# Performance work log

Hardware: AMD Instinct MI355X
Metric: run time of the kernel (lower is better)

## Reference

```python
import jax, jax.numpy as jnp
import numpy as np

DIM = 1024
D_STATE = 16
D_CONV = 4
EXPAND = 2
D_INNER = DIM * EXPAND
DT_RANK = 64  # ceil(1024/16)
N_EXP = 8
TOP_K = 2
HID = DIM * 2
B, T = 2, 2048
EPS = 1e-5


def setup_inputs() -> dict:
    key = jax.random.key(0)
    ks = jax.random.split(key, 16)
    s = 0.02
    # dt bias init (softplus-inverse of dt in [1e-3, 1e-1]) as in the torch code
    dt_init = jnp.exp(jax.random.uniform(ks[0], (D_INNER,)) * (np.log(0.1) - np.log(0.001)) + np.log(0.001))
    dt_proj_b = dt_init + jnp.log(-jnp.expm1(-dt_init))
    A_log = jnp.broadcast_to(jnp.log(jnp.arange(1, D_STATE + 1, dtype=jnp.float32))[None, :], (D_INNER, D_STATE))
    return {
        "x": jax.random.normal(ks[1], (B, T, DIM), jnp.float32),
        "ssm_state": jnp.zeros((B, D_INNER, D_STATE), jnp.float32),
        "conv_state": jnp.zeros((B, D_INNER, D_CONV - 1), jnp.float32),
        "ln1_s": jnp.ones((DIM,), jnp.float32), "ln1_b": jnp.zeros((DIM,), jnp.float32),
        "ln2_s": jnp.ones((DIM,), jnp.float32), "ln2_b": jnp.zeros((DIM,), jnp.float32),
        "in_proj_w": jax.random.normal(ks[2], (2 * D_INNER, DIM), jnp.float32) * s,
        "conv_w": jax.random.normal(ks[3], (D_INNER, 1, D_CONV), jnp.float32) * 0.2,
        "conv_b": jnp.zeros((D_INNER,), jnp.float32),
        "x_proj_w": jax.random.normal(ks[4], (DT_RANK + 2 * D_STATE, D_INNER), jnp.float32) * s,
        "dt_proj_w": jax.random.normal(ks[5], (D_INNER, DT_RANK), jnp.float32) * s,
        "dt_proj_b": dt_proj_b,
        "A_log": A_log,
        "Dp": jnp.ones((D_INNER,), jnp.float32),
        "out_proj_w": jax.random.normal(ks[6], (DIM, D_INNER), jnp.float32) * s,
        "router_w": jax.random.normal(ks[7], (N_EXP, DIM), jnp.float32) * s,
        "w_gate": jax.random.normal(ks[8], (N_EXP, HID, DIM), jnp.float32) * s,
        "w_up": jax.random.normal(ks[9], (N_EXP, HID, DIM), jnp.float32) * s,
        "w_down": jax.random.normal(ks[10], (N_EXP, DIM, HID), jnp.float32) * s,
    }


def _layernorm(x, scale, bias):
    mu = x.mean(-1, keepdims=True)
    var = ((x - mu) ** 2).mean(-1, keepdims=True)
    return (x - mu) * jax.lax.rsqrt(var + EPS) * scale + bias


def _mamba(xn, ssm_state, conv_state, in_proj_w, conv_w, conv_b, x_proj_w, dt_proj_w, dt_proj_b, A_log, Dp, out_proj_w):
    xz = jnp.einsum("btd,ed->bte", xn, in_proj_w)          # [B,T,2*di]
    x_in, z = xz[..., :D_INNER], xz[..., D_INNER:]
    # causal depthwise conv with running buffer
    xc = jnp.concatenate([conv_state, x_in.transpose(0, 2, 1)], axis=2)  # [B,di,T+dc-1]
    new_conv_state = xc[:, :, -(D_CONV - 1):]
    conv = jax.lax.conv_general_dilated(xc, conv_w, (1,), "VALID",
                                        dimension_numbers=("NCH", "OIH", "NCH"),
                                        feature_group_count=D_INNER)
    conv = conv + conv_b[None, :, None]
    xcs = jax.nn.silu(conv).transpose(0, 2, 1)              # [B,T,di]
    proj = jnp.einsum("bti,pi->btp", xcs, x_proj_w)
    dt_raw = proj[..., :DT_RANK]
    Bp = proj[..., DT_RANK:DT_RANK + D_STATE]
    Cp = proj[..., DT_RANK + D_STATE:]
    dt = jax.nn.softplus(jnp.einsum("btr,ir->bti", dt_raw, dt_proj_w) + dt_proj_b)
    A = -jnp.exp(A_log)                                     # [di,ds]

    def step(h, inp):
        dt_t, B_t, C_t, x_t = inp                           # [B,di],[B,ds],[B,ds],[B,di]
        dA = jnp.exp(dt_t[..., None] * A)                   # [B,di,ds]
        dB = dt_t[..., None] * B_t[:, None, :]
        h = dA * h + dB * x_t[..., None]
        y = jnp.sum(h * C_t[:, None, :], -1) + Dp * x_t
        return h, y

    xs = (dt.transpose(1, 0, 2), Bp.transpose(1, 0, 2), Cp.transpose(1, 0, 2), xcs.transpose(1, 0, 2))
    h, ys = jax.lax.scan(step, ssm_state, xs)
    y = ys.transpose(1, 0, 2) * jax.nn.silu(z)
    out = jnp.einsum("bti,di->btd", y, out_proj_w)
    return out, h, new_conv_state


def _moe(x, router_w, w_gate, w_up, w_down):
    Bb, Tt, D = x.shape
    xf = x.reshape(-1, D)                                   # [N,D]
    probs = jax.nn.softmax(xf @ router_w.T, axis=-1)        # [N,E]
    tw, ti = jax.lax.top_k(probs, TOP_K)
    tw = tw / tw.sum(-1, keepdims=True)
    gate = jax.nn.silu(jnp.einsum("nd,ehd->neh", xf, w_gate))
    up = jnp.einsum("nd,ehd->neh", xf, w_up)
    eo = jnp.einsum("neh,edh->ned", gate * up, w_down)      # [N,E,D]
    sel = jnp.take_along_axis(eo, ti[:, :, None], axis=1)   # [N,K,D]
    out = (tw[..., None] * sel).sum(1)
    return out.reshape(Bb, Tt, D)


def reference(x, ssm_state, conv_state, ln1_s, ln1_b, ln2_s, ln2_b, in_proj_w, conv_w, conv_b,
              x_proj_w, dt_proj_w, dt_proj_b, A_log, Dp, out_proj_w, router_w, w_gate, w_up, w_down):
    mamba_out, h, new_conv = _mamba(_layernorm(x, ln1_s, ln1_b), ssm_state, conv_state,
                                    in_proj_w, conv_w, conv_b, x_proj_w, dt_proj_w, dt_proj_b,
                                    A_log, Dp, out_proj_w)
    x1 = x + mamba_out
    out = x1 + _moe(_layernorm(x1, ln2_s, ln2_b), router_w, w_gate, w_up, w_down)
    return out
```

## Files before the change

### kernel.cpp

```cpp
#include <hip/hip_runtime.h>
#include <hip/hip_bf16.h>
#include <math.h>

#define DIM 1024
#define D_STATE 16
#define D_CONV 4
#define D_INNER 2048
#define DT_RANK 64
#define N_EXP 8
#define TOP_K 2
#define HID 2048
#define BB 2
#define TT 2048
#define NTOK (BB*TT)
#define NSLOT (NTOK*TOP_K)
#define EPS 1e-5f
#define NCHUNK 64
#define CLEN (TT/NCHUNK)

#define OFF_R0   ((size_t)0)
#define OFF_R1   ((size_t)4194304)
#define OFF_R2   ((size_t)8388608)
#define OFF_XZ   ((size_t)10485760)
#define OFF_G    ((size_t)10485760)
#define OFF_H    ((size_t)18874368)
#define OFF_XCS  ((size_t)27262976)
#define OFF_DTP  ((size_t)35651584)
#define OFF_X1   ((size_t)44040192)
#define OFF_PROJ ((size_t)48234496)
#define OFF_TW   ((size_t)48627712)
#define OFF_INT  ((size_t)48635904)
#define IO_TI    0
#define IO_CNT   8192
#define IO_CUR   8200
#define IO_OFS   8208
#define IO_TOK   8216
#define IO_SLOT  16408

typedef __attribute__((ext_vector_type(4))) float f32x4;
typedef __attribute__((ext_vector_type(8))) __bf16 bf16x8;
typedef __attribute__((ext_vector_type(4))) __bf16 bf16x4;

__device__ __forceinline__ float siluf(float v){ return v / (1.f + expf(-v)); }

__device__ __forceinline__ f32x4 mfma16(bf16x8 a, bf16x8 b, f32x4 c){
    return __builtin_amdgcn_mfma_f32_16x16x32_bf16(a, b, c, 0, 0, 0);
}

__device__ __forceinline__ void gload16(const void* g, void* l){
    __builtin_amdgcn_global_load_lds(
        (const __attribute__((address_space(1))) unsigned int*)g,
        (__attribute__((address_space(3))) unsigned int*)l, 16, 0, 0);
}

__device__ __forceinline__ void cvt_store16(__bf16* dst, f32x4 a0, f32x4 a1, f32x4 a2, f32x4 a3){
    bf16x8 p0, p1;
    #pragma unroll
    for (int j = 0; j < 4; ++j){
        p0[j]   = (__bf16)a0[j];
        p0[j+4] = (__bf16)a1[j];
        p1[j]   = (__bf16)a2[j];
        p1[j+4] = (__bf16)a3[j];
    }
    *(bf16x8*)dst = p0;
    *(bf16x8*)(dst+8) = p1;
}

__global__ __launch_bounds__(256) void cvt_w_kernel(const float* __restrict__ src,
    __bf16* __restrict__ dst, int n4)
{
    int i = blockIdx.x*256 + threadIdx.x;
    int stride = gridDim.x*256;
    for (; i < n4; i += stride){
        f32x4 v = *(const f32x4*)(src + (size_t)i*4);
        bf16x4 o;
        o[0] = (__bf16)v[0]; o[1] = (__bf16)v[1];
        o[2] = (__bf16)v[2]; o[3] = (__bf16)v[3];
        *(bf16x4*)(dst + (size_t)i*4) = o;
    }
}

template<int BOTH>
__global__ __launch_bounds__(256) void ln_kernel(const float* __restrict__ x,
    const float* __restrict__ s, const float* __restrict__ b,
    __bf16* __restrict__ obf, float* __restrict__ of32)
{
    int t = blockIdx.x;
    const float* xp = x + (size_t)t * DIM;
    float v[4]; float sum = 0.f, sq = 0.f;
    #pragma unroll
    for (int j = 0; j < 4; ++j){
        v[j] = xp[threadIdx.x + 256*j];
        sum += v[j]; sq += v[j]*v[j];
    }
    #pragma unroll
    for (int off = 32; off; off >>= 1){
        sum += __shfl_xor(sum, off, 64);
        sq  += __shfl_xor(sq , off, 64);
    }
    __shared__ float red[4][2];
    int w = threadIdx.x >> 6, lane = threadIdx.x & 63;
    if (lane == 0){ red[w][0] = sum; red[w][1] = sq; }
    __syncthreads();
    sum = red[0][0]+red[1][0]+red[2][0]+red[3][0];
    sq  = red[0][1]+red[1][1]+red[2][1]+red[3][1];
    float mu = sum * (1.f/DIM);
    float var = sq * (1.f/DIM) - mu*mu;
    float r = rsqrtf(var + EPS);
    #pragma unroll
    for (int j = 0; j < 4; ++j){
        int d = threadIdx.x + 256*j;
        float o = (v[j]-mu)*r*s[d] + b[d];
        obf[(size_t)t*DIM + d] = (__bf16)o;
        if (BOTH) of32[(size_t)t*DIM + d] = o;
    }
}

template<int MODE, int EPI, int CBF, int SWZ>
__global__ __launch_bounds__(256,3) void mfma_gemm_fast(
    const __bf16* __restrict__ A, const __bf16* __restrict__ W,
    const void* __restrict__ RG, void* __restrict__ Cv,
    const int* __restrict__ tok_of_slot, const int* __restrict__ counts,
    const int* __restrict__ offs, int M, int N, int K, int lda)
{
    int bx = blockIdx.x, by = blockIdx.y;
    if (SWZ){
        int nwg = gridDim.x*gridDim.y;
        int id = by*gridDim.x + bx;
        int swz = (id & 7)*(nwg >> 3) + (id >> 3);
        bx = swz % gridDim.x; by = swz / gridDim.x;
    }
    int e    = (MODE == 0) ? 0 : blockIdx.z;
    int cnt  = (MODE == 0) ? M : counts[e];
    int base = (MODE == 0) ? 0 : offs[e];
    int m0 = by * 128;
    if (m0 >= cnt) return;
    int n0 = bx * 128;
    const __bf16* We = W + (size_t)e * N * K;

    __shared__ __bf16 As[128*32];
    __shared__ __bf16 Ws[128*32];

    int tid = threadIdx.x;
    int wave = tid >> 6, lane = tid & 63;
    int c0 = wave*2, c1 = wave*2 + 1;
    int lr0 = c0*16 + (lane >> 2);
    int lr1 = c1*16 + (lane >> 2);
    int koff = (lane & 3) * 8;

    int ar0, ar1;
    {
        int m0c = m0 + lr0, m1c = m0 + lr1;
        if (MODE != 0){
            if (m0c >= cnt) m0c = cnt - 1;
            if (m1c >= cnt) m1c = cnt - 1;
        }
        if (MODE == 1){ ar0 = tok_of_slot[base + m0c]; ar1 = tok_of_slot[base + m1c]; }
        else if (MODE == 2){ ar0 = base + m0c; ar1 = base + m1c; }
        else { ar0 = m0c; ar1 = m1c; }
    }
    const __bf16* aS0 = A + (size_t)ar0 * lda + koff;
    const __bf16* aS1 = A + (size_t)ar1 * lda + koff;
    const __bf16* wS0 = We + (size_t)(n0 + lr0) * K + koff;
    const __bf16* wS1 = We + (size_t)(n0 + lr1) * K + koff;
    __bf16* ldsA0 = As + c0*512;
    __bf16* ldsA1 = As + c1*512;
    __bf16* ldsW0 = Ws + c0*512;
    __bf16* ldsW1 = Ws + c1*512;

    int wm = (wave >> 1) * 64, wn = (wave & 1) * 64;
    int fr = lane & 15, fk = (lane >> 4) * 8;

    f32x4 acc[4][4];
    #pragma unroll
    for (int i = 0; i < 4; ++i)
        #pragma unroll
        for (int j = 0; j < 4; ++j)
            acc[i][j] = (f32x4){0.f, 0.f, 0.f, 0.f};

    for (int k0 = 0; k0 < K; k0 += 32){
        gload16(aS0 + k0, ldsA0);
        gload16(aS1 + k0, ldsA1);
        gload16(wS0 + k0, ldsW0);
        gload16(wS1 + k0, ldsW1);
        __syncthreads();
        bf16x8 af[4], bf[4];
        #pragma unroll
        for (int i = 0; i < 4; ++i)
            af[i] = *(const bf16x8*)&As[(wm + i*16 + fr)*32 + fk];
        #pragma unroll
        for (int j = 0; j < 4; ++j)
            bf[j] = *(const bf16x8*)&Ws[(wn + j*16 + fr)*32 + fk];
        #pragma unroll
        for (int i = 0; i < 4; ++i)
            #pragma unroll
            for (int j = 0; j < 4; ++j)
                acc[i][j] = mfma16(af[i], bf[j], acc[i][j]);
        __syncthreads();
    }

    int orow = (lane >> 4) * 4;
    int ocol = lane & 15;
    #pragma unroll
    for (int i = 0; i < 4; ++i){
        #pragma unroll
        for (int jj = 0; jj < 4; ++jj){
            #pragma unroll
            for (int j = 0; j < 4; ++j){
                int m = m0 + wm + i*16 + orow + j;
                int n = n0 + wn + jj*16 + ocol;
                if (m < cnt){
                    size_t row = (size_t)(base + m);
                    float v = acc[i][jj][j];
                    if (EPI == 1) v += ((const float*)RG)[row * (size_t)N + n];
                    if (EPI == 2){
                        float g = (float)((const __bf16*)RG)[row * (size_t)N + n];
                        v = siluf(g) * v;
                    }
                    if (CBF) ((__bf16*)Cv)[row * (size_t)N + n] = (__bf16)v;
                    else     ((float* )Cv)[row * (size_t)N + n] = v;
                }
            }
        }
    }
}

template<int EPI>
__global__ __launch_bounds__(256,2) void mfma_gemm(
    const float* __restrict__ A, const float* __restrict__ W,
    const float* __restrict__ bias, float* __restrict__ C,
    int M, int N, int K, int lda)
{
    int m0 = blockIdx.y * 128;
    int n0 = blockIdx.x * 128;

    __shared__ __bf16 As[128*32];
    __shared__ __bf16 Ws[128*32];

    int tid = threadIdx.x;
    int srow = tid >> 1;
    int scol = (tid & 1) * 16;

    const float* af = A + (size_t)(m0 + srow) * lda + scol;
    int wrow = n0 + srow; if (wrow >= N) wrow = N - 1;
    const float* wptr = W + (size_t)wrow * K + scol;

    f32x4 raf[4], rw[4];
    #pragma unroll
    for (int q = 0; q < 4; ++q){
        raf[q] = *(const f32x4*)(af + q*4);
        rw[q]  = *(const f32x4*)(wptr + q*4);
    }

    int wave = tid >> 6, lane = tid & 63;
    int wm = (wave >> 1) * 64, wn = (wave & 1) * 64;
    int fr = lane & 15, fk = (lane >> 4) * 8;

    f32x4 acc[4][4];
    #pragma unroll
    for (int i = 0; i < 4; ++i)
        #pragma unroll
        for (int j = 0; j < 4; ++j)
            acc[i][j] = (f32x4){0.f, 0.f, 0.f, 0.f};

    for (int k0 = 0; k0 < K; k0 += 32){
        cvt_store16(&As[srow*32 + scol], raf[0], raf[1], raf[2], raf[3]);
        cvt_store16(&Ws[srow*32 + scol], rw[0], rw[1], rw[2], rw[3]);
        __syncthreads();
        if (k0 + 32 < K){
            #pragma unroll
            for (int q = 0; q < 4; ++q){
                raf[q] = *(const f32x4*)(af + k0 + 32 + q*4);
                rw[q]  = *(const f32x4*)(wptr + k0 + 32 + q*4);
            }
        }
        bf16x8 afr[4], bfr[4];
        #pragma unroll
        for (int i = 0; i < 4; ++i)
            afr[i] = *(const bf16x8*)&As[(wm + i*16 + fr)*32 + fk];
        #pragma unroll
        for (int i = 0; i < 4; ++i)
            bfr[i] = *(const bf16x8*)&Ws[(wn + i*16 + fr)*32 + fk];
        #pragma unroll
        for (int i = 0; i < 4; ++i)
            #pragma unroll
            for (int j = 0; j < 4; ++j)
                acc[i][j] = mfma16(afr[i], bfr[j], acc[i][j]);
        __syncthreads();
    }

    int orow = (lane >> 4) * 4;
    int ocol = lane & 15;
    #pragma unroll
    for (int i = 0; i < 4; ++i){
        #pragma unroll
        for (int jj = 0; jj < 4; ++jj){
            #pragma unroll
            for (int j = 0; j < 4; ++j){
                int m = m0 + wm + i*16 + orow + j;
                int n = n0 + wn + jj*16 + ocol;
                if (m < M && n < N){
                    float v = acc[i][jj][j];
                    if (EPI == 3){
                        v += bias[n];
                        v = (v > 20.f) ? v : log1pf(expf(v));
                    }
                    C[(size_t)m * N + n] = v;
                }
            }
        }
    }
}

__global__ __launch_bounds__(256) void conv_kernel(const float* __restrict__ xz,
    const float* __restrict__ cs, const float* __restrict__ cw,
    const float* __restrict__ cb, float* __restrict__ xcs)
{
    int idx = blockIdx.x*256 + threadIdx.x;
    int d = idx & (D_INNER-1);
    int bt = idx >> 11;
    int b = bt >> 11;
    int t = bt & (TT-1);
    float acc = cb[d];
    #pragma unroll
    for (int k = 0; k < 4; ++k){
        int tau = t + k - 3;
        float xv;
        if (tau >= 0) xv = xz[(size_t)(b*TT + tau)*(2*D_INNER) + d];
        else          xv = cs[((size_t)b*D_INNER + d)*3 + (tau + 3)];
        acc += cw[d*4 + k] * xv;
    }
    xcs[idx] = siluf(acc);
}

__global__ __launch_bounds__(256) void scan_pass1(const float* __restrict__ dtp,
    const float* __restrict__ proj, const float* __restrict__ xcs,
    const float* __restrict__ A_log, float* __restrict__ hend,
    float* __restrict__ sumdt)
{
    int gid = blockIdx.x*256 + threadIdx.x;
    int bd = gid & (BB*D_INNER-1);
    int chunk = gid >> 12;
    int b = bd >> 11, d = bd & (D_INNER-1);
    float As[D_STATE], h[D_STATE];
    #pragma unroll
    for (int s = 0; s < D_STATE; ++s){
        As[s] = -__expf(A_log[d*D_STATE + s]);
        h[s] = 0.f;
    }
    float sdt = 0.f;
    int base = b*TT + chunk*CLEN;
    for (int t = 0; t < CLEN; ++t){
        size_t bt = (size_t)(base + t);
        float dt = dtp[bt*D_INNER + d];
        float x  = xcs[bt*D_INNER + d];
        f32x4 Bv[4];
        #pragma unroll
        for (int q = 0; q < 4; ++q) Bv[q] = *(const f32x4*)(proj + bt*96 + DT_RANK + q*4);
        float dtx = dt * x;
        sdt += dt;
        #pragma unroll
        for (int s = 0; s < D_STATE; ++s)
            h[s] = __expf(dt*As[s])*h[s] + Bv[s>>2][s&3]*dtx;
    }
    size_t hb = ((size_t)bd*NCHUNK + chunk)*D_STATE;
    #pragma unroll
    for (int q = 0; q < 4; ++q)
        *(f32x4*)(hend + hb + q*4) = (f32x4){h[q*4], h[q*4+1], h[q*4+2], h[q*4+3]};
    sumdt[bd*NCHUNK + chunk] = sdt;
}

__global__ __launch_bounds__(256) void scan_combine(const float* __restrict__ hend,
    const float* __restrict__ sumdt, const float* __restrict__ A_log,
    const float* __restrict__ ssm0, float* __restrict__ hstart)
{
    int gid = blockIdx.x*256 + threadIdx.x;
    int s = gid & 15;
    int bd = gid >> 4;
    int b = bd >> 11, d = bd & (D_INNER-1);
    float As = -__expf(A_log[d*D_STATE + s]);
    float h = ssm0[((size_t)b*D_INNER + d)*D_STATE + s];
    for (int c = 0; c < NCHUNK; ++c){
        size_t idx = ((size_t)bd*NCHUNK + c)*D_STATE + s;
        hstart[idx] = h;
        h = hend[idx] + __expf(As * sumdt[bd*NCHUNK + c]) * h;
    }
}

__global__ __launch_bounds__(256) void scan_pass3(const float* __restrict__ dtp,
    const float* __restrict__ proj, const float* __restrict__ xcs,
    const float* __restrict__ xz, const float* __restrict__ A_log,
    const float* __restrict__ Dp, const float* __restrict__ hstart,
    __bf16* __restrict__ ym)
{
    int gid = blockIdx.x*256 + threadIdx.x;
    int bd = gid & (BB*D_INNER-1);
    int chunk = gid >> 12;
    int b = bd >> 11, d = bd & (D_INNER-1);
    float As[D_STATE], h[D_STATE];
    #pragma unroll
    for (int s = 0; s < D_STATE; ++s)
        As[s] = -__expf(A_log[d*D_STATE + s]);
    size_t hb = ((size_t)bd*NCHUNK + chunk)*D_STATE;
    #pragma unroll
    for (int q = 0; q < 4; ++q){
        f32x4 hv = *(const f32x4*)(hstart + hb + q*4);
        h[q*4] = hv[0]; h[q*4+1] = hv[1]; h[q*4+2] = hv[2]; h[q*4+3] = hv[3];
    }
    float Dd = Dp[d];
    int base = b*TT + chunk*CLEN;
    for (int t = 0; t < CLEN; ++t){
        size_t bt = (size_t)(base + t);
        float dt = dtp[bt*D_INNER + d];
        float x  = xcs[bt*D_INNER + d];
        f32x4 Bv[4], Cv[4];
        #pragma unroll
        for (int q = 0; q < 4; ++q){
            Bv[q] = *(const f32x4*)(proj + bt*96 + DT_RANK + q*4);
            Cv[q] = *(const f32x4*)(proj + bt*96 + DT_RANK + D_STATE + q*4);
        }
        float dtx = dt * x;
        float p = 0.f;
        #pragma unroll
        for (int s = 0; s < D_STATE; ++s){
            h[s] = __expf(dt*As[s])*h[s] + Bv[s>>2][s&3]*dtx;
            p += h[s] * Cv[s>>2][s&3];
        }
        float y = p + Dd*x;
        float z = xz[bt*(2*D_INNER) + D_INNER + d];
        float sz = z / (1.f + __expf(-z));
        ym[bt*D_INNER + d] = (__bf16)(y * sz);
    }
}

__global__ __launch_bounds__(256) void router_kernel(const float* __restrict__ xn2,
    const float* __restrict__ rw, float* __restrict__ tw, int* __restrict__ ti,
    int* __restrict__ counts)
{
    int tok = blockIdx.x*4 + (threadIdx.x >> 6);
    int lane = threadIdx.x & 63;
    float p[N_EXP] = {};
    const float* xp = xn2 + (size_t)tok * DIM;
    for (int dd = lane; dd < DIM; dd += 64){
        float xv = xp[dd];
        #pragma unroll
        for (int e = 0; e < N_EXP; ++e) p[e] += xv * rw[e*DIM + dd];
    }
    #pragma unroll
    for (int e = 0; e < N_EXP; ++e){
        #pragma unroll
        for (int off = 32; off; off >>= 1) p[e] += __shfl_xor(p[e], off, 64);
    }
    if (lane == 0){
        float mx = p[0];
        #pragma unroll
        for (int e = 1; e < N_EXP; ++e) mx = fmaxf(mx, p[e]);
        float q[N_EXP]; float ssum = 0.f;
        #pragma unroll
        for (int e = 0; e < N_EXP; ++e){ q[e] = expf(p[e]-mx); ssum += q[e]; }
        int i0 = 0;
        #pragma unroll
        for (int e = 1; e < N_EXP; ++e) if (q[e] > q[i0]) i0 = e;
        int i1 = (i0 == 0) ? 1 : 0;
        #pragma unroll
        for (int e = 0; e < N_EXP; ++e) if (e != i0 && q[e] > q[i1]) i1 = e;
        float w0 = q[i0]/ssum, w1 = q[i1]/ssum;
        float sw = w0 + w1; w0 /= sw; w1 /= sw;
        tw[tok*2] = w0; tw[tok*2+1] = w1;
        ti[tok*2] = i0; ti[tok*2+1] = i1;
        atomicAdd(&counts[i0], 1);
        atomicAdd(&counts[i1], 1);
    }
}

__global__ void offs_kernel(const int* __restrict__ counts, int* __restrict__ offs)
{
    if (threadIdx.x == 0 && blockIdx.x == 0){
        int s = 0;
        for (int e = 0; e < N_EXP; ++e){ offs[e] = s; s += counts[e]; }
    }
}

__global__ __launch_bounds__(256) void assign_kernel(const int* __restrict__ ti,
    const int* __restrict__ offs, int* __restrict__ cursors,
    int* __restrict__ tok_of_slot, int* __restrict__ slot_of)
{
    int t = blockIdx.x*256 + threadIdx.x;
    if (t >= NTOK) return;
    #pragma unroll
    for (int k = 0; k < TOP_K; ++k){
        int e = ti[t*2 + k];
        int pos = atomicAdd(&cursors[e], 1);
        int slot = offs[e] + pos;
        tok_of_slot[slot] = t;
        slot_of[t*2 + k] = slot;
    }
}

__global__ __launch_bounds__(256) void final_kernel(const float* __restrict__ x1,
    const float* __restrict__ down_out, const float* __restrict__ tw,
    const int* __restrict__ slot_of, float* __restrict__ out)
{
    int idx4 = blockIdx.x*256 + threadIdx.x;
    int t = idx4 >> 8;
    int c = idx4 & 255;
    float w0 = tw[t*2], w1 = tw[t*2+1];
    size_t s0 = (size_t)slot_of[t*2] * DIM;
    size_t s1 = (size_t)slot_of[t*2+1] * DIM;
    float4 a = *(const float4*)(x1 + (size_t)t*DIM + c*4);
    float4 d0 = *(const float4*)(down_out + s0 + c*4);
    float4 d1 = *(const float4*)(down_out + s1 + c*4);
    float4 r;
    r.x = a.x + w0*d0.x + w1*d1.x;
    r.y = a.y + w0*d0.y + w1*d1.y;
    r.z = a.z + w0*d0.z + w1*d1.z;
    r.w = a.w + w0*d0.w + w1*d1.w;
    *(float4*)(out + (size_t)t*DIM + c*4) = r;
}

extern "C" void kernel_launch(void* const* d_in, const int* in_sizes, int n_in,
                              void* d_out, int out_size, void* d_ws, size_t ws_size,
                              hipStream_t stream)
{
    const float* x        = (const float*)d_in[0];
    const float* ssm0     = (const float*)d_in[1];
    const float* conv0    = (const float*)d_in[2];
    const float* ln1_s    = (const float*)d_in[3];
    const float* ln1_b    = (const float*)d_in[4];
    const float* ln2_s    = (const float*)d_in[5];
    const float* ln2_b    = (const float*)d_in[6];
    const float* in_proj  = (const float*)d_in[7];
    const float* conv_w   = (const float*)d_in[8];
    const float* conv_b   = (const float*)d_in[9];
    const float* x_proj   = (const float*)d_in[10];
    const float* dt_proj  = (const float*)d_in[11];
    const float* dt_b     = (const float*)d_in[12];
    const float* A_log    = (const float*)d_in[13];
    const float* Dp       = (const float*)d_in[14];
    const float* out_proj = (const float*)d_in[15];
    const float* router_w = (const float*)d_in[16];
    const float* w_gate   = (const float*)d_in[17];
    const float* w_up     = (const float*)d_in[18];
    const float* w_down   = (const float*)d_in[19];
    float* out = (float*)d_out;

    float* ws = (float*)d_ws;
    __bf16* xn_bf  = (__bf16*)(ws + OFF_R0);
    float*  hend   = ws + OFF_R0;
    __bf16* ym_bf  = (__bf16*)(ws + OFF_R0);
    float*  hst    = ws + OFF_R1;
    float*  xn2f   = ws + OFF_R1;
    float*  sdt    = ws + OFF_R2;
    __bf16* opbf   = (__bf16*)(ws + OFF_R2);
    __bf16* xn2bf  = (__bf16*)(ws + OFF_R2);
    float*  xz     = ws + OFF_XZ;
    __bf16* G      = (__bf16*)(ws + OFF_G);
    __bf16* H      = (__bf16*)(ws + OFF_H);
    float*  xcs    = ws + OFF_XCS;
    float*  dnout  = ws + OFF_XCS;
    float*  dtp    = ws + OFF_DTP;
    __bf16* ipbf   = (__bf16*)(ws + OFF_DTP);
    __bf16* wbf    = (__bf16*)(ws + OFF_DTP);
    float*  x1     = ws + OFF_X1;
    float*  proj   = ws + OFF_PROJ;
    float*  tw     = ws + OFF_TW;
    int*    ip     = (int*)(ws + OFF_INT);
    int* ti          = ip + IO_TI;
    int* counts      = ip + IO_CNT;
    int* cursors     = ip + IO_CUR;
    int* offs        = ip + IO_OFS;
    int* tok_of_slot = ip + IO_TOK;
    int* slot_of     = ip + IO_SLOT;

    hipMemsetAsync(counts, 0, 16*sizeof(int), stream);

    cvt_w_kernel<<<1024, 256, 0, stream>>>(in_proj, ipbf, (2*D_INNER*DIM)/4);
    ln_kernel<0><<<NTOK, 256, 0, stream>>>(x, ln1_s, ln1_b, xn_bf, nullptr);
    mfma_gemm_fast<0,0,0,1><<<dim3(32,32), 256, 0, stream>>>(xn_bf, ipbf, nullptr, xz,
        nullptr, nullptr, nullptr, NTOK, 2*D_INNER, DIM, DIM);
    conv_kernel<<<(NTOK*D_INNER)/256, 256, 0, stream>>>(xz, conv0, conv_w, conv_b, xcs);
    mfma_gemm<0><<<dim3(1,32), 256, 0, stream>>>(xcs, x_proj, nullptr, proj,
        NTOK, 96, D_INNER, D_INNER);
    mfma_gemm<3><<<dim3(16,32), 256, 0, stream>>>(proj, dt_proj, dt_b, dtp,
        NTOK, D_INNER, DT_RANK, 96);
    scan_pass1<<<1024, 256, 0, stream>>>(dtp, proj, xcs, A_log, hend, sdt);
    scan_combine<<<256, 256, 0, stream>>>(hend, sdt, A_log, ssm0, hst);
    scan_pass3<<<1024, 256, 0, stream>>>(dtp, proj, xcs, xz, A_log, Dp, hst, ym_bf);
    cvt_w_kernel<<<512, 256, 0, stream>>>(out_proj, opbf, (DIM*D_INNER)/4);
    mfma_gemm_fast<0,1,0,1><<<dim3(8,32), 256, 0, stream>>>(ym_bf, opbf, x, x1,
        nullptr, nullptr, nullptr, NTOK, DIM, D_INNER, D_INNER);
    ln_kernel<1><<<NTOK, 256, 0, stream>>>(x1, ln2_s, ln2_b, xn2bf, xn2f);
    router_kernel<<<NTOK/4, 256, 0, stream>>>(xn2f, router_w, tw, ti, counts);
    offs_kernel<<<1, 64, 0, stream>>>(counts, offs);
    assign_kernel<<<NTOK/256, 256, 0, stream>>>(ti, offs, cursors, tok_of_slot, slot_of);
    cvt_w_kernel<<<2048, 256, 0, stream>>>(w_gate, wbf, (N_EXP*HID*DIM)/4);
    mfma_gemm_fast<1,0,1,0><<<dim3(HID/128, 64, N_EXP), 256, 0, stream>>>(xn2bf, wbf, nullptr, G,
        tok_of_slot, counts, offs, NSLOT, HID, DIM, DIM);
    cvt_w_kernel<<<2048, 256, 0, stream>>>(w_up, wbf, (N_EXP*HID*DIM)/4);
    mfma_gemm_fast<1,2,1,0><<<dim3(HID/128, 64, N_EXP), 256, 0, stream>>>(xn2bf, wbf, G, H,
        tok_of_slot, counts, offs, NSLOT, HID, DIM, DIM);
    cvt_w_kernel<<<2048, 256, 0, stream>>>(w_down, wbf, (N_EXP*DIM*HID)/4);
    mfma_gemm_fast<2,0,0,0><<<dim3(DIM/128, 64, N_EXP), 256, 0, stream>>>(H, wbf, nullptr, dnout,
        tok_of_slot, counts, offs, NSLOT, DIM, HID, HID);
    final_kernel<<<(NTOK*DIM/4)/256, 256, 0, stream>>>(x1, dnout, tw, slot_of, out);
}
```

Baseline: 841.3 us.

## Fuse gate/up MoE GEMMs, fuse LN2 with router, split-K bf16 x_proj

Gate and up expert projections are computed in one kernel that shares the gathered activation tile and applies SiLU*up in the epilogue, so the G intermediate is never written to and re-read from memory. LayerNorm2 and the router are fused, which removes the fp32 normalized-activation buffer. The x_proj GEMM now runs on a bf16 copy of the conv output with zero-padded weights and split-K (8 slices), followed by a reduction kernel, to raise parallelism over the previous 32-block launch. The fused gate/up kernel uses more registers (launch bounds drop to 2 blocks per CU), and the extra bf16 and partial-sum buffers add some traffic.

```diff
diff --git a/kernel.cpp b/kernel.cpp
--- a/kernel.cpp
+++ b/kernel.cpp
@@ -17,19 +17,22 @@
 #define EPS 1e-5f
 #define NCHUNK 64
 #define CLEN (TT/NCHUNK)
+#define XPJ_KS 8
+#define XPJ_KLEN (D_INNER/XPJ_KS)
 
 #define OFF_R0   ((size_t)0)
 #define OFF_R1   ((size_t)4194304)
 #define OFF_R2   ((size_t)8388608)
 #define OFF_XZ   ((size_t)10485760)
-#define OFF_G    ((size_t)10485760)
-#define OFF_H    ((size_t)18874368)
+#define OFF_H    OFF_XZ
+#define OFF_WU   ((size_t)18874368)
 #define OFF_XCS  ((size_t)27262976)
 #define OFF_DTP  ((size_t)35651584)
 #define OFF_X1   ((size_t)44040192)
 #define OFF_PROJ ((size_t)48234496)
 #define OFF_TW   ((size_t)48627712)
 #define OFF_INT  ((size_t)48635904)
+#define OFF_XPW  ((size_t)48668672)
 #define IO_TI    0
 #define IO_CNT   8192
 #define IO_CUR   8200
@@ -80,10 +83,27 @@
     }
 }
 
-template<int BOTH>
+__global__ __launch_bounds__(256) void cvt_pad_xproj(const float* __restrict__ src,
+    __bf16* __restrict__ dst)
+{
+    int i = blockIdx.x*256 + threadIdx.x;
+    int base = i*4;
+    int row = base >> 11;
+    bf16x4 o;
+    if (row < 96){
+        f32x4 v = *(const f32x4*)(src + base);
+        o[0] = (__bf16)v[0]; o[1] = (__bf16)v[1];
+        o[2] = (__bf16)v[2]; o[3] = (__bf16)v[3];
+    } else {
+        o[0] = (__bf16)0.f; o[1] = (__bf16)0.f;
+        o[2] = (__bf16)0.f; o[3] = (__bf16)0.f;
+    }
+    *(bf16x4*)(dst + base) = o;
+}
+
 __global__ __launch_bounds__(256) void ln_kernel(const float* __restrict__ x,
     const float* __restrict__ s, const float* __restrict__ b,
-    __bf16* __restrict__ obf, float* __restrict__ of32)
+    __bf16* __restrict__ obf)
 {
     int t = blockIdx.x;
     const float* xp = x + (size_t)t * DIM;
@@ -110,9 +130,80 @@
     #pragma unroll
     for (int j = 0; j < 4; ++j){
         int d = threadIdx.x + 256*j;
+        obf[(size_t)t*DIM + d] = (__bf16)((v[j]-mu)*r*s[d] + b[d]);
+    }
+}
+
+__global__ __launch_bounds__(256) void ln2_router_kernel(const float* __restrict__ x,
+    const float* __restrict__ s, const float* __restrict__ b,
+    const float* __restrict__ rw, __bf16* __restrict__ obf,
+    float* __restrict__ tw, int* __restrict__ ti, int* __restrict__ counts)
+{
+    int t = blockIdx.x;
+    const float* xp = x + (size_t)t * DIM;
+    float v[4]; float sum = 0.f, sq = 0.f;
+    #pragma unroll
+    for (int j = 0; j < 4; ++j){
+        v[j] = xp[threadIdx.x + 256*j];
+        sum += v[j]; sq += v[j]*v[j];
+    }
+    #pragma unroll
+    for (int off = 32; off; off >>= 1){
+        sum += __shfl_xor(sum, off, 64);
+        sq  += __shfl_xor(sq , off, 64);
+    }
+    __shared__ float red[4][2];
+    __shared__ float red2[4][N_EXP];
+    int w = threadIdx.x >> 6, lane = threadIdx.x & 63;
+    if (lane == 0){ red[w][0] = sum; red[w][1] = sq; }
+    __syncthreads();
+    sum = red[0][0]+red[1][0]+red[2][0]+red[3][0];
+    sq  = red[0][1]+red[1][1]+red[2][1]+red[3][1];
+    float mu = sum * (1.f/DIM);
+    float var = sq * (1.f/DIM) - mu*mu;
+    float r = rsqrtf(var + EPS);
+    float p[N_EXP] = {};
+    #pragma unroll
+    for (int j = 0; j < 4; ++j){
+        int d = threadIdx.x + 256*j;
         float o = (v[j]-mu)*r*s[d] + b[d];
         obf[(size_t)t*DIM + d] = (__bf16)o;
-        if (BOTH) of32[(size_t)t*DIM + d] = o;
+        #pragma unroll
+        for (int e = 0; e < N_EXP; ++e) p[e] += o * rw[e*DIM + d];
+    }
+    #pragma unroll
+    for (int e = 0; e < N_EXP; ++e){
+        #pragma unroll
+        for (int off = 32; off; off >>= 1) p[e] += __shfl_xor(p[e], off, 64);
+    }
+    if (lane == 0){
+        #pragma unroll
+        for (int e = 0; e < N_EXP; ++e) red2[w][e] = p[e];
+    }
+    __syncthreads();
+    if (threadIdx.x == 0){
+        float q[N_EXP];
+        #pragma unroll
+        for (int e = 0; e < N_EXP; ++e)
+            q[e] = red2[0][e]+red2[1][e]+red2[2][e]+red2[3][e];
+        float mx = q[0];
+        #pragma unroll
+        for (int e = 1; e < N_EXP; ++e) mx = fmaxf(mx, q[e]);
+        float ssum = 0.f;
+        #pragma unroll
+        for (int e = 0; e < N_EXP; ++e){ q[e] = expf(q[e]-mx); ssum += q[e]; }
+        int i0 = 0;
+        #pragma unroll
+        for (int e = 1; e < N_EXP; ++e) if (q[e] > q[i0]) i0 = e;
+        int i1 = (i0 == 0) ? 1 : 0;
+        #pragma unroll
+        for (int e = 0; e < N_EXP; ++e) if (e != i0 && q[e] > q[i1]) i1 = e;
+        float w0 = q[i0]/ssum, w1 = q[i1]/ssum;
+        float sw = w0 + w1; w0 /= sw; w1 /= sw;
+        tw[t*2] = w0; tw[t*2+1] = w1;
+        ti[t*2] = i0; ti[t*2+1] = i1;
+        atomicAdd(&counts[i0], 1);
+        atomicAdd(&counts[i1], 1);
     }
 }
 
@@ -213,10 +304,6 @@
                     size_t row = (size_t)(base + m);
                     float v = acc[i][jj][j];
                     if (EPI == 1) v += ((const float*)RG)[row * (size_t)N + n];
-                    if (EPI == 2){
-                        float g = (float)((const __bf16*)RG)[row * (size_t)N + n];
-                        v = siluf(g) * v;
-                    }
                     if (CBF) ((__bf16*)Cv)[row * (size_t)N + n] = (__bf16)v;
                     else     ((float* )Cv)[row * (size_t)N + n] = v;
                 }
@@ -225,8 +312,195 @@
     }
 }
 
-template<int EPI>
-__global__ __launch_bounds__(256,2) void mfma_gemm(
+__global__ __launch_bounds__(256,2) void moe_gateup_fast(
+    const __bf16* __restrict__ A, const __bf16* __restrict__ Wg,
+    const __bf16* __restrict__ Wu, const int* __restrict__ tok_of_slot,
+    const int* __restrict__ counts, const int* __restrict__ offs,
+    __bf16* __restrict__ H)
+{
+    int e = blockIdx.z;
+    int cnt = counts[e];
+    int base = offs[e];
+    int m0 = blockIdx.y * 128;
+    if (m0 >= cnt) return;
+    int n0 = blockIdx.x * 128;
+    const __bf16* Wge = Wg + (size_t)e * HID * DIM;
+    const __bf16* Wue = Wu + (size_t)e * HID * DIM;
+
+    __shared__ __bf16 As[128*32];
+    __shared__ __bf16 Gs[128*32];
+    __shared__ __bf16 Us[128*32];
+
+    int tid = threadIdx.x;
+    int wave = tid >> 6, lane = tid & 63;
+    int c0 = wave*2, c1 = wave*2 + 1;
+    int lr0 = c0*16 + (lane >> 2);
+    int lr1 = c1*16 + (lane >> 2);
+    int koff = (lane & 3) * 8;
+
+    int m0c = m0 + lr0, m1c = m0 + lr1;
+    if (m0c >= cnt) m0c = cnt - 1;
+    if (m1c >= cnt) m1c = cnt - 1;
+    int ar0 = tok_of_slot[base + m0c];
+    int ar1 = tok_of_slot[base + m1c];
+
+    const __bf16* aS0 = A + (size_t)ar0 * DIM + koff;
+    const __bf16* aS1 = A + (size_t)ar1 * DIM + koff;
+    const __bf16* gS0 = Wge + (size_t)(n0 + lr0) * DIM + koff;
+    const __bf16* gS1 = Wge + (size_t)(n0 + lr1) * DIM + koff;
+    const __bf16* uS0 = Wue + (size_t)(n0 + lr0) * DIM + koff;
+    const __bf16* uS1 = Wue + (size_t)(n0 + lr1) * DIM + koff;
+    __bf16* ldsA0 = As + c0*512;
+    __bf16* ldsA1 = As + c1*512;
+    __bf16* ldsG0 = Gs + c0*512;
+    __bf16* ldsG1 = Gs + c1*512;
+    __bf16* ldsU0 = Us + c0*512;
+    __bf16* ldsU1 = Us + c1*512;
+
+    int wm = (wave >> 1) * 64, wn = (wave & 1) * 64;
+    int fr = lane & 15, fk = (lane >> 4) * 8;
+
+    f32x4 accg[4][4], accu[4][4];
+    #pragma unroll
+    for (int i = 0; i < 4; ++i)
+        #pragma unroll
+        for (int j = 0; j < 4; ++j){
+            accg[i][j] = (f32x4){0.f, 0.f, 0.f, 0.f};
+            accu[i][j] = (f32x4){0.f, 0.f, 0.f, 0.f};
+        }
+
+    for (int k0 = 0; k0 < DIM; k0 += 32){
+        gload16(aS0 + k0, ldsA0);
+        gload16(aS1 + k0, ldsA1);
+        gload16(gS0 + k0, ldsG0);
+        gload16(gS1 + k0, ldsG1);
+        gload16(uS0 + k0, ldsU0);
+        gload16(uS1 + k0, ldsU1);
+        __syncthreads();
+        bf16x8 af[4], gf[4], uf[4];
+        #pragma unroll
+        for (int i = 0; i < 4; ++i){
+            af[i] = *(const bf16x8*)&As[(wm + i*16 + fr)*32 + fk];
+            gf[i] = *(const bf16x8*)&Gs[(wn + i*16 + fr)*32 + fk];
+            uf[i] = *(const bf16x8*)&Us[(wn + i*16 + fr)*32 + fk];
+        }
+        #pragma unroll
+        for (int i = 0; i < 4; ++i)
+            #pragma unroll
+            for (int j = 0; j < 4; ++j){
+                accg[i][j] = mfma16(af[i], gf[j], accg[i][j]);
+                accu[i][j] = mfma16(af[i], uf[j], accu[i][j]);
+            }
+        __syncthreads();
+    }
+
+    int orow = (lane >> 4) * 4;
+    int ocol = lane & 15;
+    #pragma unroll
+    for (int i = 0; i < 4; ++i){
+        #pragma unroll
+        for (int jj = 0; jj < 4; ++jj){
+            #pragma unroll
+            for (int j = 0; j < 4; ++j){
+                int m = m0 + wm + i*16 + orow + j;
+                if (m < cnt){
+                    int n = n0 + wn + jj*16 + ocol;
+                    size_t row = (size_t)(base + m);
+                    float g = accg[i][jj][j], u = accu[i][jj][j];
+                    H[row * (size_t)HID + n] = (__bf16)(siluf(g) * u);
+                }
+            }
+        }
+    }
+}
+
+__global__ __launch_bounds__(256,3) void xproj_ks_kernel(
+    const __bf16* __restrict__ A, const __bf16* __restrict__ W,
+    float* __restrict__ Cpart)
+{
+    int m0 = blockIdx.y * 128;
+    int kbeg = blockIdx.z * XPJ_KLEN;
+
+    __shared__ __bf16 As[128*32];
+    __shared__ __bf16 Ws[128*32];
+
+    int tid = threadIdx.x;
+    int wave = tid >> 6, lane = tid & 63;
+    int c0 = wave*2, c1 = wave*2 + 1;
+    int lr0 = c0*16 + (lane >> 2);
+    int lr1 = c1*16 + (lane >> 2);
+    int koff = (lane & 3) * 8;
+
+    const __bf16* aS0 = A + (size_t)(m0 + lr0) * D_INNER + kbeg + koff;
+    const __bf16* aS1 = A + (size_t)(m0 + lr1) * D_INNER + kbeg + koff;
+    const __bf16* wS0 = W + (size_t)lr0 * D_INNER + kbeg + koff;
+    const __bf16* wS1 = W + (size_t)lr1 * D_INNER + kbeg + koff;
+    __bf16* ldsA0 = As + c0*512;
+    __bf16* ldsA1 = As + c1*512;
+    __bf16* ldsW0 = Ws + c0*512;
+    __bf16* ldsW1 = Ws + c1*512;
+
+    int wm = (wave >> 1) * 64, wn = (wave & 1) * 64;
+    int fr = lane & 15, fk = (lane >> 4) * 8;
+
+    f32x4 acc[4][4];
+    #pragma unroll
+    for (int i = 0; i < 4; ++i)
+        #pragma unroll
+        for (int j = 0; j < 4; ++j)
+            acc[i][j] = (f32x4){0.f, 0.f, 0.f, 0.f};
+
+    for (int k0 = 0; k0 < XPJ_KLEN; k0 += 32){
+        gload16(aS0 + k0, ldsA0);
+        gload16(aS1 + k0, ldsA1);
+        gload16(wS0 + k0, ldsW0);
+        gload16(wS1 + k0, ldsW1);
+        __syncthreads();
+        bf16x8 af[4], bf[4];
+        #pragma unroll
+        for (int i = 0; i < 4; ++i)
+            af[i] = *(const bf16x8*)&As[(wm + i*16 + fr)*32 + fk];
+        #pragma unroll
+        for (int j = 0; j < 4; ++j)
+            bf[j] = *(const bf16x8*)&Ws[(wn + j*16 + fr)*32 + fk];
+        #pragma unroll
+        for (int i = 0; i < 4; ++i)
+            #pragma unroll
+            for (int j = 0; j < 4; ++j)
+                acc[i][j] = mfma16(af[i], bf[j], acc[i][j]);
+        __syncthreads();
+    }
+
+    float* Cz = Cpart + (size_t)blockIdx.z * NTOK * 128;
+    int orow = (lane >> 4) * 4;
+    int ocol = lane & 15;
+    #pragma unroll
+    for (int i = 0; i < 4; ++i){
+        #pragma unroll
+        for (int jj = 0; jj < 4; ++jj){
+            #pragma unroll
+            for (int j = 0; j < 4; ++j){
+                int m = m0 + wm + i*16 + orow + j;
+                int n = wn + jj*16 + ocol;
+                Cz[(size_t)m * 128 + n] = acc[i][jj][j];
+            }
+        }
+    }
+}
+
+__global__ __launch_bounds__(256) void xproj_reduce(const float* __restrict__ Cpart,
+    float* __restrict__ proj)
+{
+    int idx = blockIdx.x*256 + threadIdx.x;
+    int t = idx / 96, n = idx - t*96;
+    float s = 0.f;
+    #pragma unroll
+    for (int z = 0; z < XPJ_KS; ++z)
+        s += Cpart[(size_t)z * NTOK * 128 + (size_t)t * 128 + n];
+    proj[idx] = s;
+}
+
+__global__ __launch_bounds__(256,2) void dt_gemm(
     const float* __restrict__ A, const float* __restrict__ W,
     const float* __restrict__ bias, float* __restrict__ C,
     int M, int N, int K, int lda)
@@ -242,8 +516,7 @@
     int scol = (tid & 1) * 16;
 
     const float* af = A + (size_t)(m0 + srow) * lda + scol;
-    int wrow = n0 + srow; if (wrow >= N) wrow = N - 1;
-    const float* wptr = W + (size_t)wrow * K + scol;
+    const float* wptr = W + (size_t)(n0 + srow) * K + scol;
 
     f32x4 raf[4], rw[4];
     #pragma unroll
@@ -300,11 +573,8 @@
                 int m = m0 + wm + i*16 + orow + j;
                 int n = n0 + wn + jj*16 + ocol;
                 if (m < M && n < N){
-                    float v = acc[i][jj][j];
-                    if (EPI == 3){
-                        v += bias[n];
-                        v = (v > 20.f) ? v : log1pf(expf(v));
-                    }
+                    float v = acc[i][jj][j] + bias[n];
+                    v = (v > 20.f) ? v : log1pf(expf(v));
                     C[(size_t)m * N + n] = v;
                 }
             }
@@ -314,7 +584,8 @@
 
 __global__ __launch_bounds__(256) void conv_kernel(const float* __restrict__ xz,
     const float* __restrict__ cs, const float* __restrict__ cw,
-    const float* __restrict__ cb, float* __restrict__ xcs)
+    const float* __restrict__ cb, float* __restrict__ xcs,
+    __bf16* __restrict__ xcs_bf)
 {
     int idx = blockIdx.x*256 + threadIdx.x;
     int d = idx & (D_INNER-1);
@@ -330,7 +601,9 @@
         else          xv = cs[((size_t)b*D_INNER + d)*3 + (tau + 3)];
         acc += cw[d*4 + k] * xv;
     }
-    xcs[idx] = siluf(acc);
+    float v = siluf(acc);
+    xcs[idx] = v;
+    xcs_bf[idx] = (__bf16)v;
 }
 
 __global__ __launch_bounds__(256) void scan_pass1(const float* __restrict__ dtp,
@@ -430,46 +703,6 @@
         float z = xz[bt*(2*D_INNER) + D_INNER + d];
         float sz = z / (1.f + __expf(-z));
         ym[bt*D_INNER + d] = (__bf16)(y * sz);
-    }
-}
-
-__global__ __launch_bounds__(256) void router_kernel(const float* __restrict__ xn2,
-    const float* __restrict__ rw, float* __restrict__ tw, int* __restrict__ ti,
-    int* __restrict__ counts)
-{
-    int tok = blockIdx.x*4 + (threadIdx.x >> 6);
-    int lane = threadIdx.x & 63;
-    float p[N_EXP] = {};
-    const float* xp = xn2 + (size_t)tok * DIM;
-    for (int dd = lane; dd < DIM; dd += 64){
-        float xv = xp[dd];
-        #pragma unroll
-        for (int e = 0; e < N_EXP; ++e) p[e] += xv * rw[e*DIM + dd];
-    }
-    #pragma unroll
-    for (int e = 0; e < N_EXP; ++e){
-        #pragma unroll
-        for (int off = 32; off; off >>= 1) p[e] += __shfl_xor(p[e], off, 64);
-    }
-    if (lane == 0){
-        float mx = p[0];
-        #pragma unroll
-        for (int e = 1; e < N_EXP; ++e) mx = fmaxf(mx, p[e]);
-        float q[N_EXP]; float ssum = 0.f;
-        #pragma unroll
-        for (int e = 0; e < N_EXP; ++e){ q[e] = expf(p[e]-mx); ssum += q[e]; }
-        int i0 = 0;
-        #pragma unroll
-        for (int e = 1; e < N_EXP; ++e) if (q[e] > q[i0]) i0 = e;
-        int i1 = (i0 == 0) ? 1 : 0;
-        #pragma unroll
-        for (int e = 0; e < N_EXP; ++e) if (e != i0 && q[e] > q[i1]) i1 = e;
-        float w0 = q[i0]/ssum, w1 = q[i1]/ssum;
-        float sw = w0 + w1; w0 /= sw; w1 /= sw;
-        tw[tok*2] = w0; tw[tok*2+1] = w1;
-        ti[tok*2] = i0; ti[tok*2+1] = i1;
-        atomicAdd(&counts[i0], 1);
-        atomicAdd(&counts[i1], 1);
     }
 }
 
@@ -548,22 +781,25 @@
     __bf16* xn_bf  = (__bf16*)(ws + OFF_R0);
     float*  hend   = ws + OFF_R0;
     __bf16* ym_bf  = (__bf16*)(ws + OFF_R0);
+    float*  xpart  = ws + OFF_R1;
     float*  hst    = ws + OFF_R1;
-    float*  xn2f   = ws + OFF_R1;
     float*  sdt    = ws + OFF_R2;
     __bf16* opbf   = (__bf16*)(ws + OFF_R2);
     __bf16* xn2bf  = (__bf16*)(ws + OFF_R2);
     float*  xz     = ws + OFF_XZ;
-    __bf16* G      = (__bf16*)(ws + OFF_G);
     __bf16* H      = (__bf16*)(ws + OFF_H);
+    __bf16* wubf   = (__bf16*)(ws + OFF_WU);
     float*  xcs    = ws + OFF_XCS;
     float*  dnout  = ws + OFF_XCS;
     float*  dtp    = ws + OFF_DTP;
     __bf16* ipbf   = (__bf16*)(ws + OFF_DTP);
-    __bf16* wbf    = (__bf16*)(ws + OFF_DTP);
+    __bf16* wgbf   = (__bf16*)(ws + OFF_DTP);
+    __bf16* wdbf   = (__bf16*)(ws + OFF_DTP);
+    __bf16* xcs_bf = (__bf16*)(ws + OFF_X1);
     float*  x1     = ws + OFF_X1;
     float*  proj   = ws + OFF_PROJ;
     float*  tw     = ws + OFF_TW;
+    __bf16* xpw    = (__bf16*)(ws + OFF_XPW);
     int*    ip     = (int*)(ws + OFF_INT);
     int* ti          = ip + IO_TI;
     int* counts      = ip + IO_CNT;
@@ -575,13 +811,14 @@
     hipMemsetAsync(counts, 0, 16*sizeof(int), stream);
 
     cvt_w_kernel<<<1024, 256, 0, stream>>>(in_proj, ipbf, (2*D_INNER*DIM)/4);
-    ln_kernel<0><<<NTOK, 256, 0, stream>>>(x, ln1_s, ln1_b, xn_bf, nullptr);
+    ln_kernel<<<NTOK, 256, 0, stream>>>(x, ln1_s, ln1_b, xn_bf);
     mfma_gemm_fast<0,0,0,1><<<dim3(32,32), 256, 0, stream>>>(xn_bf, ipbf, nullptr, xz,
         nullptr, nullptr, nullptr, NTOK, 2*D_INNER, DIM, DIM);
-    conv_kernel<<<(NTOK*D_INNER)/256, 256, 0, stream>>>(xz, conv0, conv_w, conv_b, xcs);
-    mfma_gemm<0><<<dim3(1,32), 256, 0, stream>>>(xcs, x_proj, nullptr, proj,
-        NTOK, 96, D_INNER, D_INNER);
-    mfma_gemm<3><<<dim3(16,32), 256, 0, stream>>>(proj, dt_proj, dt_b, dtp,
+    conv_kernel<<<(NTOK*D_INNER)/256, 256, 0, stream>>>(xz, conv0, conv_w, conv_b, xcs, xcs_bf);
+    cvt_pad_xproj<<<256, 256, 0, stream>>>(x_proj, xpw);
+    xproj_ks_kernel<<<dim3(1,32,XPJ_KS), 256, 0, stream>>>(xcs_bf, xpw, xpart);
+    xproj_reduce<<<(NTOK*96)/256, 256, 0, stream>>>(xpart, proj);
+    dt_gemm<<<dim3(16,32), 256, 0, stream>>>(proj, dt_proj, dt_b, dtp,
         NTOK, D_INNER, DT_RANK, 96);
     scan_pass1<<<1024, 256, 0, stream>>>(dtp, proj, xcs, A_log, hend, sdt);
     scan_combine<<<256, 256, 0, stream>>>(hend, sdt, A_log, ssm0, hst);
@@ -589,18 +826,16 @@
     cvt_w_kernel<<<512, 256, 0, stream>>>(out_proj, opbf, (DIM*D_INNER)/4);
     mfma_gemm_fast<0,1,0,1><<<dim3(8,32), 256, 0, stream>>>(ym_bf, opbf, x, x1,
         nullptr, nullptr, nullptr, NTOK, DIM, D_INNER, D_INNER);
-    ln_kernel<1><<<NTOK, 256, 0, stream>>>(x1, ln2_s, ln2_b, xn2bf, xn2f);
-    router_kernel<<<NTOK/4, 256, 0, stream>>>(xn2f, router_w, tw, ti, counts);
+    ln2_router_kernel<<<NTOK, 256, 0, stream>>>(x1, ln2_s, ln2_b, router_w,
+        xn2bf, tw, ti, counts);
     offs_kernel<<<1, 64, 0, stream>>>(counts, offs);
     assign_kernel<<<NTOK/256, 256, 0, stream>>>(ti, offs, cursors, tok_of_slot, slot_of);
-    cvt_w_kernel<<<2048, 256, 0, stream>>>(w_gate, wbf, (N_EXP*HID*DIM)/4);
-    mfma_gemm_fast<1,0,1,0><<<dim3(HID/128, 64, N_EXP), 256, 0, stream>>>(xn2bf, wbf, nullptr, G,
-        tok_of_slot, counts, offs, NSLOT, HID, DIM, DIM);
-    cvt_w_kernel<<<2048, 256, 0, stream>>>(w_up, wbf, (N_EXP*HID*DIM)/4);
-    mfma_gemm_fast<1,2,1,0><<<dim3(HID/128, 64, N_EXP), 256, 0, stream>>>(xn2bf, wbf, G, H,
-        tok_of_slot, counts, offs, NSLOT, HID, DIM, DIM);
-    cvt_w_kernel<<<2048, 256, 0, stream>>>(w_down, wbf, (N_EXP*DIM*HID)/4);
-    mfma_gemm_fast<2,0,0,0><<<dim3(DIM/128, 64, N_EXP), 256, 0, stream>>>(H, wbf, nullptr, dnout,
+    cvt_w_kernel<<<2048, 256, 0, stream>>>(w_gate, wgbf, (N_EXP*HID*DIM)/4);
+    cvt_w_kernel<<<2048, 256, 0, stream>>>(w_up, wubf, (N_EXP*HID*DIM)/4);
+    moe_gateup_fast<<<dim3(HID/128, 64, N_EXP), 256, 0, stream>>>(xn2bf, wgbf, wubf,
+        tok_of_slot, counts, offs, H);
+    cvt_w_kernel<<<2048, 256, 0, stream>>>(w_down, wdbf, (N_EXP*DIM*HID)/4);
+    mfma_gemm_fast<2,0,0,0><<<dim3(DIM/128, 64, N_EXP), 256, 0, stream>>>(H, wdbf, nullptr, dnout,
         tok_of_slot, counts, offs, NSLOT, DIM, HID, HID);
     final_kernel<<<(NTOK*DIM/4)/256, 256, 0, stream>>>(x1, dnout, tw, slot_of, out);
 }
```

Measured after the change: 744.3 us. 11.5% less time.
